# Kernel tuning notes

Measured on AMD Instinct MI355X. Metric: run time of the kernel, lower is better.

Reference implementation:

```python
import jax, jax.numpy as jnp
import numpy as np
import math

B, S, E, H, D, L, HF = 8, 1024, 512, 8, 64, 6, 2048
EPS = 1e-5
INF = 1000000.0


def _gelu(x):
    # custom tanh-approx gelu from the source
    return 0.5 * x * (1 + jnp.tanh(math.sqrt(2 / math.pi) * (x + 0.044715 * x ** 3)))


def _layernorm(x, gamma, beta):
    mean = jnp.mean(x, axis=-1, keepdims=True)
    var = jnp.mean((x - mean) ** 2, axis=-1, keepdims=True)
    return gamma * ((x - mean) / jnp.sqrt(var + EPS)) + beta


def setup_inputs() -> dict:
    key = jax.random.key(0)
    ks = jax.random.split(key, 10)
    scale = 0.02
    x = jax.random.normal(ks[0], (B, S, E), dtype=jnp.float32)
    att_mask = jax.random.randint(ks[1], (B, S), 0, 2) == 1
    WQ = jax.random.normal(ks[2], (L, E, E), dtype=jnp.float32) * scale
    WK = jax.random.normal(ks[3], (L, E, E), dtype=jnp.float32) * scale
    WV = jax.random.normal(ks[4], (L, E, E), dtype=jnp.float32) * scale
    WO = jax.random.normal(ks[5], (L, E, E), dtype=jnp.float32) * scale
    W1 = jax.random.normal(ks[6], (L, HF, E), dtype=jnp.float32) * scale
    W2 = jax.random.normal(ks[7], (L, E, HF), dtype=jnp.float32) * scale
    bQ = jnp.zeros((L, E)); bK = jnp.zeros((L, E)); bV = jnp.zeros((L, E)); bO = jnp.zeros((L, E))
    b1 = jnp.zeros((L, HF)); b2 = jnp.zeros((L, E))
    g1 = jnp.ones((L, E)); bt1 = jnp.zeros((L, E))
    g2 = jnp.ones((L, E)); bt2 = jnp.zeros((L, E))
    return {"x": x, "att_mask": att_mask, "WQ": WQ, "bQ": bQ, "WK": WK, "bK": bK,
            "WV": WV, "bV": bV, "WO": WO, "bO": bO, "W1": W1, "b1": b1, "W2": W2,
            "b2": b2, "g1": g1, "bt1": bt1, "g2": g2, "bt2": bt2}


def reference(x, att_mask, WQ, bQ, WK, bK, WV, bV, WO, bO, W1, b1, W2, b2, g1, bt1, g2, bt2):
    # additive mask applied to scores: score - (~mask) * infinity, broadcast over (B,1,1,S)
    inv_att = (~att_mask).astype(x.dtype)[:, None, None, :] * INF
    inv_sqrt_d = 1.0 / math.sqrt(D)
    for l in range(L):
        # --- multi-head self-attention ---
        q = (jnp.einsum('bse,fe->bsf', x, WQ[l]) + bQ[l]).reshape(B, S, H, D).transpose(0, 2, 1, 3)
        k = (jnp.einsum('bse,fe->bsf', x, WK[l]) + bK[l]).reshape(B, S, H, D).transpose(0, 2, 1, 3)
        v = (jnp.einsum('bse,fe->bsf', x, WV[l]) + bV[l]).reshape(B, S, H, D).transpose(0, 2, 1, 3)
        score = jnp.einsum('bhsd,bhtd->bhst', q, k) * inv_sqrt_d - inv_att
        attn = jax.nn.softmax(score, axis=-1)
        o = jnp.einsum('bhst,bhtd->bhsd', attn, v).transpose(0, 2, 1, 3).reshape(B, S, E)
        o = jnp.einsum('bse,fe->bsf', o, WO[l]) + bO[l]
        x = _layernorm(x + o, g1[l], bt1[l])
        # --- pointwise feed-forward ---
        h = _gelu(jnp.einsum('bse,fe->bsf', x, W1[l]) + b1[l])
        f = jnp.einsum('bsf,ef->bse', h, W2[l]) + b2[l]
        x = _layernorm(x + f, g2[l], bt2[l])
    return x
```

## Files before the change

kernel.cpp:

```cpp
#include <hip/hip_runtime.h>
#include <cstdint>
#include <cstddef>

#define NB 8
#define NS 1024
#define NE 512
#define NH 8
#define ND 64
#define NL 6
#define NHF 2048
#define NROW (NB*NS)

typedef __bf16 bf16_t;
typedef __bf16 bf8v __attribute__((ext_vector_type(8)));
typedef __bf16 bf4v __attribute__((ext_vector_type(4)));
typedef float  f4   __attribute__((ext_vector_type(4)));

extern "C" __device__ float __ocml_native_exp2_f32(float);
#define EXP2F __ocml_native_exp2_f32
#define LOG2E 1.4426950408889634f

__device__ __forceinline__ void async_copy16(const bf16_t* g, bf16_t* l) {
    __builtin_amdgcn_global_load_lds(
        (const __attribute__((address_space(1))) void*)g,
        (__attribute__((address_space(3))) void*)l,
        16, 0, 0);
}

__device__ __forceinline__ float gelu_f(float x) {
    const float s = fmaf(0.044715f * x * x, x, x);
    const float e = EXP2F(-2.3022081995f * s);
    return x * __builtin_amdgcn_rcpf(1.0f + e);
}

template<int BN, int ACT, int OUT>
__device__ __forceinline__ void gemm_core(
    bf16_t* __restrict__ sm,
    const bf16_t* __restrict__ A, const bf16_t* __restrict__ Bm,
    const float* __restrict__ bias, bf16_t* __restrict__ Cb,
    const unsigned short* __restrict__ rank,
    int m0, int n0, int N, int K)
{
    constexpr int JN = BN / 32, WSPAN = BN / 2;
    bf16_t* As = sm;
    bf16_t* Bs = sm + 2*128*64;
    const int tid  = threadIdx.x;
    const int lane = tid & 63;
    const int wave = tid >> 6;
    const int wm = wave >> 1, wn = wave & 1;
    const int quad = lane >> 4, l16 = lane & 15;
    const int srow = tid >> 3;
    const int scol = (((tid & 7) ^ (srow & 7)) << 3);

    f4 acc[4][JN] = {};

    const bf16_t* Ag = A  + (size_t)(m0 + srow) * K + scol;
    const bf16_t* Bg = Bm + (size_t)(n0 + srow) * K + scol;
    const int sw = (l16 & 7);

    auto stage = [&](int buf, int kt) {
#pragma unroll
        for (int r = 0; r < 4; ++r)
            async_copy16(Ag + (size_t)r * 32 * K + kt, As + buf*8192 + tid*8 + r*2048);
#pragma unroll
        for (int r = 0; r < BN/32; ++r)
            async_copy16(Bg + (size_t)r * 32 * K + kt, Bs + buf*(BN*64) + tid*8 + r*2048);
    };

    stage(0, 0);
    int buf = 0;
    for (int kt = 0; kt < K; kt += 64, buf ^= 1) {
        __syncthreads();
        if (kt + 64 < K) stage(buf ^ 1, kt + 64);
        const bf16_t* Ab = As + buf*8192;
        const bf16_t* Bb = Bs + buf*(BN*64);
#pragma unroll
        for (int s = 0; s < 2; ++s) {
            const int c8 = ((s*4 + quad) ^ sw) * 8;
            bf8v af[4], bfv[JN];
#pragma unroll
            for (int i = 0; i < 4; ++i)
                af[i] = *(const bf8v*)(Ab + (wm*64 + i*16 + l16)*64 + c8);
#pragma unroll
            for (int j = 0; j < JN; ++j)
                bfv[j] = *(const bf8v*)(Bb + (wn*WSPAN + j*16 + l16)*64 + c8);
#pragma unroll
            for (int i = 0; i < 4; ++i)
#pragma unroll
                for (int j = 0; j < JN; ++j) {
                    if (OUT == 5)
                        acc[i][j] = __builtin_amdgcn_mfma_f32_16x16x32_bf16(af[i], bfv[j], acc[i][j], 0, 0, 0);
                    else
                        acc[i][j] = __builtin_amdgcn_mfma_f32_16x16x32_bf16(bfv[j], af[i], acc[i][j], 0, 0, 0);
                }
        }
    }

    if (OUT != 5) {
#pragma unroll
        for (int i = 0; i < 4; ++i) {
            const int mi = m0 + wm*64 + i*16 + l16;
            size_t m = (size_t)mi;
            if (OUT == 4) m = (size_t)((mi & ~1023) + (int)rank[mi]);
#pragma unroll
            for (int j = 0; j < JN; ++j) {
                const int nb = n0 + wn*WSPAN + j*16 + quad*4;
                const f4 bv = *(const f4*)(bias + nb);
                f4 v = acc[i][j] + bv;
                if (ACT) {
#pragma unroll
                    for (int r = 0; r < 4; ++r) v[r] = gelu_f(v[r]);
                }
                bf4v* cp = (bf4v*)(Cb + m * (size_t)N + nb);
                bf4v o;
                if (OUT == 2) {
                    const bf4v old = *cp;
#pragma unroll
                    for (int r = 0; r < 4; ++r) o[r] = (bf16_t)((float)old[r] + v[r]);
                } else {
#pragma unroll
                    for (int r = 0; r < 4; ++r) o[r] = (bf16_t)v[r];
                }
                *cp = o;
            }
        }
    } else {
#pragma unroll
        for (int j = 0; j < JN; ++j) {
            const int n = n0 + wn*WSPAN + j*16 + l16;
            const float bv = bias[n];
#pragma unroll
            for (int i = 0; i < 4; ++i) {
                const int mbase = m0 + wm*64 + i*16 + quad*4;
                const size_t b8h = (size_t)((mbase >> 10)*8 + (n >> 6));
                bf16_t* rowp = Cb + (b8h*64 + (size_t)(n & 63))*1024;
#pragma unroll
                for (int r = 0; r < 4; ++r)
                    rowp[rank[mbase + r]] = (bf16_t)(acc[i][j][r] + bv);
            }
        }
    }
}

template<int BN, int ACT, int OUT>
__global__ __launch_bounds__(256)
void gemm_bt_k(const bf16_t* __restrict__ A, const bf16_t* __restrict__ Bm,
               const float* __restrict__ bias, bf16_t* __restrict__ Cb, int N, int K)
{
    __shared__ __align__(16) bf16_t smem[2*128*64 + 2*BN*64];
    gemm_core<BN, ACT, OUT>(smem, A, Bm, bias, Cb, nullptr,
                            blockIdx.x * 128, blockIdx.y * BN, N, K);
}

template<int ACT, int OUT>
__device__ __forceinline__ void gemm256_core(
    bf16_t* __restrict__ sm,
    const bf16_t* __restrict__ A, const bf16_t* __restrict__ Bm,
    const float* __restrict__ bias, bf16_t* __restrict__ Cb,
    const unsigned short* __restrict__ rank,
    int m0, int n0, int N, int K)
{
    const int tid  = threadIdx.x;
    const int lane = tid & 63;
    const int wave = tid >> 6;
    const int wm = wave >> 2, wn = wave & 3;
    const int quad = lane >> 4, l16 = lane & 15;
    const int sw = l16 & 7;
    const int srow = tid >> 3;
    const int scol = ((tid & 7) ^ (srow & 7)) << 3;

    bf16_t* As = sm;
    bf16_t* Bs = sm + 4 * 8192;

    const bf16_t* Ag = A  + (size_t)(m0 + srow) * K + scol;
    const bf16_t* Bg = Bm + (size_t)(n0 + srow) * K + scol;

    auto stageA = [&](int d, int h, int kt) {
        bf16_t* dst = As + (d*2 + h) * 8192 + tid * 8;
        const bf16_t* src = Ag + (size_t)(h * 128) * K + kt;
        async_copy16(src, dst);
        async_copy16(src + (size_t)64 * K, dst + 4096);
    };
    auto stageB = [&](int d, int h, int kt) {
        bf16_t* dst = Bs + (d*2 + h) * 8192 + tid * 8;
        const bf16_t* src = Bg + (size_t)(h * 128) * K + kt;
        async_copy16(src, dst);
        async_copy16(src + (size_t)64 * K, dst + 4096);
    };

    const int nt = K >> 6;

    f4 acc[8][4] = {};
    bf8v bfr[4][2], al[4][2], ah[4][2];

    auto mfmaQ = [&](const bf8v (&af)[4][2], int fb, int gb) {
#pragma unroll
        for (int kh = 0; kh < 2; ++kh)
#pragma unroll
            for (int f = 0; f < 4; ++f)
#pragma unroll
                for (int g = 0; g < 2; ++g) {
                    if (OUT == 5)
                        acc[fb+f][gb+g] = __builtin_amdgcn_mfma_f32_16x16x32_bf16(af[f][kh], bfr[gb+g][kh], acc[fb+f][gb+g], 0, 0, 0);
                    else
                        acc[fb+f][gb+g] = __builtin_amdgcn_mfma_f32_16x16x32_bf16(bfr[gb+g][kh], af[f][kh], acc[fb+f][gb+g], 0, 0, 0);
                }
    };

    stageB(0, 0, 0);  stageB(0, 1, 0);  stageA(0, 0, 0);  stageA(0, 1, 0);
    stageB(1, 0, 64); stageB(1, 1, 64); stageA(1, 0, 64);
    asm volatile("s_waitcnt vmcnt(6)" ::: "memory");
    __builtin_amdgcn_s_barrier();

    for (int t = 0; t < nt; ++t) {
        const int d = t & 1;
        const int kt2 = (t + 2) << 6;
        const bf16_t* Ab = As + (d*2 + wm) * 8192;
        const bf16_t* Bb = Bs + (d*2 + (wn >> 1)) * 8192 + (wn & 1) * 4096;

#pragma unroll
        for (int g = 0; g < 4; ++g)
#pragma unroll
            for (int kh = 0; kh < 2; ++kh)
                bfr[g][kh] = *(const bf8v*)(Bb + (g*16 + l16)*64 + (((kh*4 + quad) ^ sw) << 3));
#pragma unroll
        for (int f = 0; f < 4; ++f)
#pragma unroll
            for (int kh = 0; kh < 2; ++kh)
                al[f][kh] = *(const bf8v*)(Ab + (f*16 + l16)*64 + (((kh*4 + quad) ^ sw) << 3));
        if (t + 1 < nt) stageA(d ^ 1, 1, (t + 1) << 6);
        __builtin_amdgcn_s_barrier();
        __builtin_amdgcn_s_setprio(1);
        mfmaQ(al, 0, 0);
        __builtin_amdgcn_s_setprio(0);
        asm volatile("s_waitcnt lgkmcnt(0)" ::: "memory");
        __builtin_amdgcn_s_barrier();

#pragma unroll
        for (int f = 0; f < 4; ++f)
#pragma unroll
            for (int kh = 0; kh < 2; ++kh)
                ah[f][kh] = *(const bf8v*)(Ab + ((f + 4)*16 + l16)*64 + (((kh*4 + quad) ^ sw) << 3));
        if (t + 2 < nt) stageB(d, 0, kt2);
        __builtin_amdgcn_s_barrier();
        __builtin_amdgcn_s_setprio(1);
        mfmaQ(ah, 4, 0);
        __builtin_amdgcn_s_setprio(0);
        asm volatile("s_waitcnt lgkmcnt(0)" ::: "memory");
        __builtin_amdgcn_s_barrier();

        if (t + 2 < nt) stageB(d, 1, kt2);
        __builtin_amdgcn_s_barrier();
        __builtin_amdgcn_s_setprio(1);
        mfmaQ(al, 0, 2);
        __builtin_amdgcn_s_setprio(0);
        asm volatile("s_waitcnt lgkmcnt(0)" ::: "memory");
        __builtin_amdgcn_s_barrier();

        if (t + 2 < nt) stageA(d, 0, kt2);
        __builtin_amdgcn_s_barrier();
        __builtin_amdgcn_s_setprio(1);
        mfmaQ(ah, 4, 2);
        __builtin_amdgcn_s_setprio(0);
        asm volatile("s_waitcnt lgkmcnt(0)" ::: "memory");
        if (t + 1 < nt) {
            if (t + 2 < nt) asm volatile("s_waitcnt vmcnt(6)" ::: "memory");
            else            asm volatile("s_waitcnt vmcnt(0)" ::: "memory");
        }
        __builtin_amdgcn_s_barrier();
    }

    if (OUT != 5) {
#pragma unroll
        for (int f = 0; f < 8; ++f) {
            const int mi = m0 + wm*128 + f*16 + l16;
            size_t m = (size_t)mi;
            if (OUT == 4) m = (size_t)((mi & ~1023) + (int)rank[mi]);
#pragma unroll
            for (int g = 0; g < 4; ++g) {
                const int nb = n0 + wn*64 + g*16 + quad*4;
                const f4 bv = *(const f4*)(bias + nb);
                f4 v = acc[f][g] + bv;
                if (ACT) {
#pragma unroll
                    for (int r = 0; r < 4; ++r) v[r] = gelu_f(v[r]);
                }
                bf4v* cp = (bf4v*)(Cb + m * (size_t)N + nb);
                bf4v o;
                if (OUT == 2) {
                    const bf4v old = *cp;
#pragma unroll
                    for (int r = 0; r < 4; ++r) o[r] = (bf16_t)((float)old[r] + v[r]);
                } else {
#pragma unroll
                    for (int r = 0; r < 4; ++r) o[r] = (bf16_t)v[r];
                }
                *cp = o;
            }
        }
    } else {
#pragma unroll
        for (int g = 0; g < 4; ++g) {
            const int n = n0 + wn*64 + g*16 + l16;
            const float bv = bias[n];
#pragma unroll
            for (int f = 0; f < 8; ++f) {
                const int mbase = m0 + wm*128 + f*16 + quad*4;
                const size_t b8h = (size_t)((mbase >> 10)*8 + (n >> 6));
                bf16_t* rowp = Cb + (b8h*64 + (size_t)(n & 63))*1024;
#pragma unroll
                for (int r = 0; r < 4; ++r)
                    rowp[rank[mbase + r]] = (bf16_t)(acc[f][g][r] + bv);
            }
        }
    }
}

template<int ACT, int OUT>
__global__ __launch_bounds__(512, 2)
void gemm256_k(const bf16_t* __restrict__ A, const bf16_t* __restrict__ Bm,
               const float* __restrict__ bias, bf16_t* __restrict__ Cb, int N, int K)
{
    __shared__ __align__(16) bf16_t smem[8 * 8192];
    gemm256_core<ACT, OUT>(smem, A, Bm, bias, Cb, nullptr,
                           blockIdx.x * 256, blockIdx.y * 256, N, K);
}

__global__ __launch_bounds__(512, 2)
void gemm256_qkv_k(const bf16_t* __restrict__ A,
                   const bf16_t* __restrict__ wq, const bf16_t* __restrict__ wk, const bf16_t* __restrict__ wv,
                   const float* __restrict__ bq, const float* __restrict__ bk, const float* __restrict__ bv,
                   bf16_t* __restrict__ Q, bf16_t* __restrict__ K, bf16_t* __restrict__ Vt,
                   const unsigned short* __restrict__ rank)
{
    __shared__ __align__(16) bf16_t smem[8 * 8192];
    const int mat = blockIdx.y >> 1;
    const int m0 = blockIdx.x * 256, n0 = (blockIdx.y & 1) * 256;
    if (mat == 0)      gemm256_core<0, 1>(smem, A, wq, bq, Q,  nullptr, m0, n0, NE, NE);
    else if (mat == 1) gemm256_core<0, 4>(smem, A, wk, bk, K,  rank,    m0, n0, NE, NE);
    else               gemm256_core<0, 5>(smem, A, wv, bv, Vt, rank,    m0, n0, NE, NE);
}

__global__ __launch_bounds__(64)
void pack_k(const int* __restrict__ m, unsigned short* __restrict__ rank,
            int* __restrict__ cntpad, float* __restrict__ maskp)
{
    const int b = blockIdx.x, lane = threadIdx.x;
    unsigned long long bals[16];
    int cnt = 0;
#pragma unroll
    for (int c = 0; c < 16; ++c) {
        const bool mk = m[b*NS + c*64 + lane] != 0;
        bals[c] = __ballot(mk);
        cnt += __popcll(bals[c]);
    }
    int u = 0, kk = 0;
#pragma unroll
    for (int c = 0; c < 16; ++c) {
        const unsigned long long bal = bals[c];
        const bool mk = (bal >> lane) & 1;
        const int pu = __popcll(bal & ((1ull << lane) - 1));
        const int r = mk ? (u + pu) : (cnt + kk + (lane - pu));
        rank[b*NS + c*64 + lane] = (unsigned short)r;
        const int cb = __popcll(bal);
        u += cb; kk += 64 - cb;
    }
    if (lane == 0) {
        int cp = (cnt + 63) & ~63;
        cntpad[b] = cp < 64 ? 64 : cp;
    }
#pragma unroll
    for (int c = 0; c < 16; ++c) {
        const int j = c*64 + lane;
        maskp[b*NS + j] = (j < cnt) ? 0.0f : -1.0e6f * LOG2E;
    }
}

__global__ __launch_bounds__(256)
void attn_k(const bf16_t* __restrict__ Q, const bf16_t* __restrict__ Kg,
            const bf16_t* __restrict__ Vt, const float* __restrict__ maskf,
            const int* __restrict__ cntpad, bf16_t* __restrict__ O)
{
    __shared__ __align__(16) bf16_t Ks[2][64*64];
    __shared__ __align__(16) bf16_t Vs[2][64*64];
    __shared__ __align__(16) bf16_t Ps[4][32*64];
    const int tid  = threadIdx.x;
    const int lane = tid & 63;
    const int wave = tid >> 6;
    const int quad = lane >> 4, l16 = lane & 15;
    const int sw = l16 & 7;
    const int bh = blockIdx.x;
    const int b = bh >> 3, h = bh & 7;
    const int q0 = blockIdx.y * 128;
    const int kend = cntpad[b];

    bf8v qf[2][2];
#pragma unroll
    for (int qi = 0; qi < 2; ++qi) {
        const bf16_t* Qp = Q + (size_t)(b*NS + q0 + wave*32 + qi*16 + l16) * NE + h*ND;
        qf[qi][0] = *(const bf8v*)(Qp + quad*8);
        qf[qi][1] = *(const bf8v*)(Qp + 32 + quad*8);
    }

    f4 oacc[2][4] = {};
    float rs[2] = {0.f, 0.f};

    const int srow = tid >> 3;
    const int scol = (((tid & 7) ^ (srow & 7)) << 3);
    const float c1 = 0.125f * LOG2E;

    auto stage = [&](int buf, int kt) {
#pragma unroll
        for (int r = 0; r < 2; ++r) {
            async_copy16(Kg + (size_t)(b*NS + kt + r*32 + srow) * NE + h*ND + scol,
                         Ks[buf] + (r*256 + tid) * 8);
            async_copy16(Vt + (size_t)(bh*ND + r*32 + srow) * NS + kt + scol,
                         Vs[buf] + (r*256 + tid) * 8);
        }
    };

    stage(0, 0);
    int buf = 0;
    for (int kt = 0; kt < kend; kt += 64, buf ^= 1) {
        __syncthreads();
        if (kt + 64 < kend) stage(buf ^ 1, kt + 64);

        f4 sacc[2][4] = {};
        __builtin_amdgcn_s_setprio(1);
#pragma unroll
        for (int j = 0; j < 4; ++j) {
            bf8v kf0 = *(const bf8v*)(Ks[buf] + (j*16 + l16)*64 + ((quad    ) ^ sw)*8);
            bf8v kf1 = *(const bf8v*)(Ks[buf] + (j*16 + l16)*64 + ((quad + 4) ^ sw)*8);
#pragma unroll
            for (int qi = 0; qi < 2; ++qi) {
                sacc[qi][j] = __builtin_amdgcn_mfma_f32_16x16x32_bf16(kf0, qf[qi][0], sacc[qi][j], 0, 0, 0);
                sacc[qi][j] = __builtin_amdgcn_mfma_f32_16x16x32_bf16(kf1, qf[qi][1], sacc[qi][j], 0, 0, 0);
            }
        }
        __builtin_amdgcn_s_setprio(0);

        bf16_t* Pw = Ps[wave];
#pragma unroll
        for (int j = 0; j < 4; ++j) {
            const f4 mkv = *(const f4*)(maskf + b*NS + kt + j*16 + quad*4);
#pragma unroll
            for (int qi = 0; qi < 2; ++qi) {
                bf4v o;
#pragma unroll
                for (int r = 0; r < 4; ++r) {
                    const float p = EXP2F(fmaf(sacc[qi][j][r], c1, mkv[r]));
                    rs[qi] += p;
                    o[r] = (bf16_t)p;
                }
                const int row = qi*16 + l16;
                const int chunk = (j*2 + (quad >> 1)) ^ sw;
                *(bf4v*)(Pw + row*64 + chunk*8 + (quad & 1)*4) = o;
            }
        }

        __builtin_amdgcn_s_setprio(1);
#pragma unroll
        for (int ks = 0; ks < 2; ++ks) {
            bf8v pf[2];
#pragma unroll
            for (int qi = 0; qi < 2; ++qi)
                pf[qi] = *(const bf8v*)(Pw + (qi*16 + l16)*64 + ((ks*4 + quad) ^ sw)*8);
#pragma unroll
            for (int nt = 0; nt < 4; ++nt) {
                bf8v vf = *(const bf8v*)(Vs[buf] + (nt*16 + l16)*64 + ((ks*4 + quad) ^ sw)*8);
#pragma unroll
                for (int qi = 0; qi < 2; ++qi)
                    oacc[qi][nt] = __builtin_amdgcn_mfma_f32_16x16x32_bf16(vf, pf[qi], oacc[qi][nt], 0, 0, 0);
            }
        }
        __builtin_amdgcn_s_setprio(0);
    }

#pragma unroll
    for (int qi = 0; qi < 2; ++qi) {
        float s = rs[qi];
        s += __shfl_xor(s, 16, 64);
        s += __shfl_xor(s, 32, 64);
        const float inv = 1.0f / s;
        const size_t row = (size_t)(b*NS + q0 + wave*32 + qi*16 + l16);
#pragma unroll
        for (int nt = 0; nt < 4; ++nt) {
            bf4v o;
#pragma unroll
            for (int r = 0; r < 4; ++r) o[r] = (bf16_t)(oacc[qi][nt][r] * inv);
            *(bf4v*)(O + row * NE + h*ND + nt*16 + quad*4) = o;
        }
    }
}

__global__ __launch_bounds__(256)
void ln_k(bf16_t* __restrict__ xb,
          const float* __restrict__ gamma, const float* __restrict__ beta,
          float* __restrict__ fout, int wf)
{
    const int row = blockIdx.x;
    const int tid = threadIdx.x;
    const size_t base = (size_t)row * NE;
    const float x0 = (float)xb[base + tid];
    const float x1 = (float)xb[base + tid + 256];
    float s  = x0 + x1;
    float ss = x0*x0 + x1*x1;
#pragma unroll
    for (int off = 32; off > 0; off >>= 1) {
        s  += __shfl_down(s,  off, 64);
        ss += __shfl_down(ss, off, 64);
    }
    __shared__ float red[8];
    const int wave = tid >> 6;
    if ((tid & 63) == 0) { red[wave] = s; red[4 + wave] = ss; }
    __syncthreads();
    s  = red[0] + red[1] + red[2] + red[3];
    ss = red[4] + red[5] + red[6] + red[7];
    const float mean = s * (1.0f / NE);
    const float var  = ss * (1.0f / NE) - mean * mean;
    const float inv  = rsqrtf(var + 1e-5f);
    const float o0 = gamma[tid]       * ((x0 - mean) * inv) + beta[tid];
    const float o1 = gamma[tid + 256] * ((x1 - mean) * inv) + beta[tid + 256];
    xb[base + tid]       = (bf16_t)o0;
    xb[base + tid + 256] = (bf16_t)o1;
    if (wf) {
        fout[base + tid]       = o0;
        fout[base + tid + 256] = o1;
    }
}

#define W4SZ ((size_t)NL*NE*NE/4)
#define WBSZ ((size_t)NL*NE*NHF/4)
#define XSZ  ((size_t)NROW*NE/4)
#define CVT_TOTAL (4*W4SZ + 2*WBSZ + XSZ)

__global__ void cvt_all(const float* __restrict__ wq, const float* __restrict__ wk,
                        const float* __restrict__ wv, const float* __restrict__ wo,
                        const float* __restrict__ w1, const float* __restrict__ w2,
                        const float* __restrict__ x,
                        bf16_t* __restrict__ owq, bf16_t* __restrict__ owk,
                        bf16_t* __restrict__ owv, bf16_t* __restrict__ owo,
                        bf16_t* __restrict__ ow1, bf16_t* __restrict__ ow2,
                        bf16_t* __restrict__ ox)
{
    size_t i = (size_t)blockIdx.x * 256 + threadIdx.x;
    if (i >= CVT_TOTAL) return;
    const float* src; bf16_t* dst;
    if      (i < 1*W4SZ)           { src = wq; dst = owq; }
    else if (i < 2*W4SZ)           { src = wk; dst = owk; i -= 1*W4SZ; }
    else if (i < 3*W4SZ)           { src = wv; dst = owv; i -= 2*W4SZ; }
    else if (i < 4*W4SZ)           { src = wo; dst = owo; i -= 3*W4SZ; }
    else if (i < 4*W4SZ + WBSZ)    { src = w1; dst = ow1; i -= 4*W4SZ; }
    else if (i < 4*W4SZ + 2*WBSZ)  { src = w2; dst = ow2; i -= 4*W4SZ + WBSZ; }
    else                           { src = x;  dst = ox;  i -= 4*W4SZ + 2*WBSZ; }
    const f4 v = ((const f4*)src)[i];
    bf4v o;
    o[0] = (bf16_t)v[0]; o[1] = (bf16_t)v[1]; o[2] = (bf16_t)v[2]; o[3] = (bf16_t)v[3];
    ((bf4v*)dst)[i] = o;
}

extern "C" void kernel_launch(void* const* d_in, const int* in_sizes, int n_in,
                              void* d_out, int out_size, void* d_ws, size_t ws_size,
                              hipStream_t stream)
{
    (void)in_sizes; (void)n_in; (void)out_size; (void)ws_size;
    const float* x   = (const float*)d_in[0];
    const int*   msk = (const int*)d_in[1];
    const float* WQ = (const float*)d_in[2];  const float* bQ  = (const float*)d_in[3];
    const float* WK = (const float*)d_in[4];  const float* bK  = (const float*)d_in[5];
    const float* WV = (const float*)d_in[6];  const float* bV  = (const float*)d_in[7];
    const float* WO = (const float*)d_in[8];  const float* bO  = (const float*)d_in[9];
    const float* W1 = (const float*)d_in[10]; const float* b1  = (const float*)d_in[11];
    const float* W2 = (const float*)d_in[12]; const float* b2  = (const float*)d_in[13];
    const float* g1 = (const float*)d_in[14]; const float* bt1 = (const float*)d_in[15];
    const float* g2 = (const float*)d_in[16]; const float* bt2 = (const float*)d_in[17];

    char* ws = (char*)d_ws;
    size_t off = 0;
    auto alloc = [&](size_t bytes) { char* p = ws + off; off += (bytes + 255) & ~(size_t)255; return p; };
    bf16_t* xb    = (bf16_t*)alloc((size_t)NROW*NE*2);
    bf16_t* Qb    = (bf16_t*)alloc((size_t)NROW*NE*2);
    bf16_t* Kb    = (bf16_t*)alloc((size_t)NROW*NE*2);
    bf16_t* Vtb   = (bf16_t*)alloc((size_t)NROW*NE*2);
    bf16_t* AOb   = (bf16_t*)alloc((size_t)NROW*NE*2);
    bf16_t* hb    = (bf16_t*)alloc((size_t)NROW*NHF*2);
    bf16_t* wqc   = (bf16_t*)alloc((size_t)NL*NE*NE*2);
    bf16_t* wkc   = (bf16_t*)alloc((size_t)NL*NE*NE*2);
    bf16_t* wvc   = (bf16_t*)alloc((size_t)NL*NE*NE*2);
    bf16_t* woc   = (bf16_t*)alloc((size_t)NL*NE*NE*2);
    bf16_t* w1c   = (bf16_t*)alloc((size_t)NL*NHF*NE*2);
    bf16_t* w2c   = (bf16_t*)alloc((size_t)NL*NE*NHF*2);
    float*  maskp = (float*) alloc((size_t)NB*NS*4);
    unsigned short* rankb = (unsigned short*)alloc((size_t)NB*NS*2);
    int*    cntp  = (int*)   alloc(NB*4);

    cvt_all<<<dim3((unsigned)((CVT_TOTAL + 255) / 256)), dim3(256), 0, stream>>>(
        WQ, WK, WV, WO, W1, W2, x, wqc, wkc, wvc, woc, w1c, w2c, xb);
    pack_k<<<dim3(NB), dim3(64), 0, stream>>>(msk, rankb, cntp, maskp);

    for (int l = 0; l < NL; ++l) {
        const bf16_t* wq  = wqc + (size_t)l*NE*NE;
        const bf16_t* wk  = wkc + (size_t)l*NE*NE;
        const bf16_t* wv  = wvc + (size_t)l*NE*NE;
        const bf16_t* wo  = woc + (size_t)l*NE*NE;
        const bf16_t* w1p = w1c + (size_t)l*NHF*NE;
        const bf16_t* w2p = w2c + (size_t)l*NE*NHF;

        gemm256_qkv_k<<<dim3(32, 6), dim3(512), 0, stream>>>(
            xb, wq, wk, wv, bQ + l*NE, bK + l*NE, bV + l*NE, Qb, Kb, Vtb, rankb);
        attn_k<<<dim3(64, 8), dim3(256), 0, stream>>>(Qb, Kb, Vtb, maskp, cntp, AOb);
        gemm_bt_k<64, 0, 2><<<dim3(64, 8), dim3(256), 0, stream>>>(
            AOb, wo, bO + l*NE, xb, NE, NE);
        ln_k<<<dim3(NROW), dim3(256), 0, stream>>>(
            xb, g1 + l*NE, bt1 + l*NE, nullptr, 0);
        gemm256_k<1, 1><<<dim3(32, 8), dim3(512), 0, stream>>>(
            xb, w1p, b1 + l*NHF, hb, NHF, NE);
        gemm_bt_k<64, 0, 2><<<dim3(64, 8), dim3(256), 0, stream>>>(
            hb, w2p, b2 + l*NE, xb, NE, NHF);
        const int last = (l == NL - 1);
        ln_k<<<dim3(NROW), dim3(256), 0, stream>>>(
            xb, g2 + l*NE, bt2 + l*NE, (float*)d_out, last);
    }
}
```

Baseline: 1.039 ms.

## Split QKV into 128-tile GEMM plus separate V transpose kernel

Replaces the 256x256-tile fused QKV GEMM, whose V output went through a scattered per-element transposed store, with a 128x128-tile GEMM over 768 blocks. That GEMM writes V row-major (rank-permuted) into a new buffer. A new LDS-based transpose kernel then builds the V^T layout that attention expects, and it skips tiles beyond the padded count. The aim is to remove the uncoalesced 2-byte scatter writes and to give the grid more blocks. The cost is an extra kernel launch and an extra read and write of V.

New measurement: 949.8 us. -8.6%, faster.

```diff
diff --git a/kernel.cpp b/kernel.cpp
--- a/kernel.cpp
+++ b/kernel.cpp
@@ -87,57 +87,36 @@
 #pragma unroll
             for (int i = 0; i < 4; ++i)
 #pragma unroll
-                for (int j = 0; j < JN; ++j) {
-                    if (OUT == 5)
-                        acc[i][j] = __builtin_amdgcn_mfma_f32_16x16x32_bf16(af[i], bfv[j], acc[i][j], 0, 0, 0);
-                    else
-                        acc[i][j] = __builtin_amdgcn_mfma_f32_16x16x32_bf16(bfv[j], af[i], acc[i][j], 0, 0, 0);
-                }
-        }
-    }
-
-    if (OUT != 5) {
-#pragma unroll
-        for (int i = 0; i < 4; ++i) {
-            const int mi = m0 + wm*64 + i*16 + l16;
-            size_t m = (size_t)mi;
-            if (OUT == 4) m = (size_t)((mi & ~1023) + (int)rank[mi]);
-#pragma unroll
-            for (int j = 0; j < JN; ++j) {
-                const int nb = n0 + wn*WSPAN + j*16 + quad*4;
-                const f4 bv = *(const f4*)(bias + nb);
-                f4 v = acc[i][j] + bv;
-                if (ACT) {
-#pragma unroll
-                    for (int r = 0; r < 4; ++r) v[r] = gelu_f(v[r]);
-                }
-                bf4v* cp = (bf4v*)(Cb + m * (size_t)N + nb);
-                bf4v o;
-                if (OUT == 2) {
-                    const bf4v old = *cp;
-#pragma unroll
-                    for (int r = 0; r < 4; ++r) o[r] = (bf16_t)((float)old[r] + v[r]);
-                } else {
-#pragma unroll
-                    for (int r = 0; r < 4; ++r) o[r] = (bf16_t)v[r];
-                }
-                *cp = o;
+                for (int j = 0; j < JN; ++j)
+                    acc[i][j] = __builtin_amdgcn_mfma_f32_16x16x32_bf16(bfv[j], af[i], acc[i][j], 0, 0, 0);
+        }
+    }
+
+#pragma unroll
+    for (int i = 0; i < 4; ++i) {
+        const int mi = m0 + wm*64 + i*16 + l16;
+        size_t m = (size_t)mi;
+        if (OUT == 4) m = (size_t)((mi & ~1023) + (int)rank[mi]);
+#pragma unroll
+        for (int j = 0; j < JN; ++j) {
+            const int nb = n0 + wn*WSPAN + j*16 + quad*4;
+            const f4 bv = *(const f4*)(bias + nb);
+            f4 v = acc[i][j] + bv;
+            if (ACT) {
+#pragma unroll
+                for (int r = 0; r < 4; ++r) v[r] = gelu_f(v[r]);
             }
-        }
-    } else {
-#pragma unroll
-        for (int j = 0; j < JN; ++j) {
-            const int n = n0 + wn*WSPAN + j*16 + l16;
-            const float bv = bias[n];
-#pragma unroll
-            for (int i = 0; i < 4; ++i) {
-                const int mbase = m0 + wm*64 + i*16 + quad*4;
-                const size_t b8h = (size_t)((mbase >> 10)*8 + (n >> 6));
-                bf16_t* rowp = Cb + (b8h*64 + (size_t)(n & 63))*1024;
-#pragma unroll
-                for (int r = 0; r < 4; ++r)
-                    rowp[rank[mbase + r]] = (bf16_t)(acc[i][j][r] + bv);
+            bf4v* cp = (bf4v*)(Cb + m * (size_t)N + nb);
+            bf4v o;
+            if (OUT == 2) {
+                const bf4v old = *cp;
+#pragma unroll
+                for (int r = 0; r < 4; ++r) o[r] = (bf16_t)((float)old[r] + v[r]);
+            } else {
+#pragma unroll
+                for (int r = 0; r < 4; ++r) o[r] = (bf16_t)v[r];
             }
+            *cp = o;
         }
     }
 }
@@ -150,6 +129,49 @@
     __shared__ __align__(16) bf16_t smem[2*128*64 + 2*BN*64];
     gemm_core<BN, ACT, OUT>(smem, A, Bm, bias, Cb, nullptr,
                             blockIdx.x * 128, blockIdx.y * BN, N, K);
+}
+
+__global__ __launch_bounds__(256)
+void gemm_qkv_k(const bf16_t* __restrict__ A,
+                const bf16_t* __restrict__ wq, const bf16_t* __restrict__ wk, const bf16_t* __restrict__ wv,
+                const float* __restrict__ bq, const float* __restrict__ bk, const float* __restrict__ bv,
+                bf16_t* __restrict__ Q, bf16_t* __restrict__ K, bf16_t* __restrict__ Vp,
+                const unsigned short* __restrict__ rank)
+{
+    __shared__ __align__(16) bf16_t smem[2*128*64 + 2*128*64];
+    const int mat = blockIdx.y >> 2;
+    const int m0 = blockIdx.x * 128, n0 = (blockIdx.y & 3) * 128;
+    if (mat == 0)      gemm_core<128, 0, 1>(smem, A, wq, bq, Q,  nullptr, m0, n0, NE, NE);
+    else if (mat == 1) gemm_core<128, 0, 4>(smem, A, wk, bk, K,  rank,    m0, n0, NE, NE);
+    else               gemm_core<128, 0, 4>(smem, A, wv, bv, Vp, rank,    m0, n0, NE, NE);
+}
+
+__global__ __launch_bounds__(256)
+void vtp_k(const bf16_t* __restrict__ Vp, const int* __restrict__ cntpad,
+           bf16_t* __restrict__ Vt)
+{
+    const int bh = blockIdx.x, b = bh >> 3, h = bh & 7;
+    const int j0 = blockIdx.y * 64;
+    if (j0 >= cntpad[b]) return;
+    __shared__ __align__(16) bf16_t t[64][72];
+    const int tid = threadIdx.x;
+    const int jr = tid >> 3;
+    const int c8 = (tid & 7) * 8;
+#pragma unroll
+    for (int r = 0; r < 2; ++r) {
+        const int j = jr + r*32;
+        *(bf8v*)(&t[j][c8]) =
+            *(const bf8v*)(Vp + (size_t)(b*NS + j0 + j) * NE + h*ND + c8);
+    }
+    __syncthreads();
+#pragma unroll
+    for (int r = 0; r < 2; ++r) {
+        const int d = jr + r*32;
+        bf8v o;
+#pragma unroll
+        for (int u = 0; u < 8; ++u) o[u] = t[c8 + u][d];
+        *(bf8v*)(Vt + (size_t)(bh*ND + d) * NS + j0 + c8) = o;
+    }
 }
 
 template<int ACT, int OUT>
@@ -157,7 +179,6 @@
     bf16_t* __restrict__ sm,
     const bf16_t* __restrict__ A, const bf16_t* __restrict__ Bm,
     const float* __restrict__ bias, bf16_t* __restrict__ Cb,
-    const unsigned short* __restrict__ rank,
     int m0, int n0, int N, int K)
 {
     const int tid  = threadIdx.x;
@@ -199,12 +220,8 @@
 #pragma unroll
             for (int f = 0; f < 4; ++f)
 #pragma unroll
-                for (int g = 0; g < 2; ++g) {
-                    if (OUT == 5)
-                        acc[fb+f][gb+g] = __builtin_amdgcn_mfma_f32_16x16x32_bf16(af[f][kh], bfr[gb+g][kh], acc[fb+f][gb+g], 0, 0, 0);
-                    else
-                        acc[fb+f][gb+g] = __builtin_amdgcn_mfma_f32_16x16x32_bf16(bfr[gb+g][kh], af[f][kh], acc[fb+f][gb+g], 0, 0, 0);
-                }
+                for (int g = 0; g < 2; ++g)
+                    acc[fb+f][gb+g] = __builtin_amdgcn_mfma_f32_16x16x32_bf16(bfr[gb+g][kh], af[f][kh], acc[fb+f][gb+g], 0, 0, 0);
     };
 
     stageB(0, 0, 0);  stageB(0, 1, 0);  stageA(0, 0, 0);  stageA(0, 1, 0);
@@ -270,48 +287,30 @@
         __builtin_amdgcn_s_barrier();
     }
 
-    if (OUT != 5) {
-#pragma unroll
-        for (int f = 0; f < 8; ++f) {
-            const int mi = m0 + wm*128 + f*16 + l16;
-            size_t m = (size_t)mi;
-            if (OUT == 4) m = (size_t)((mi & ~1023) + (int)rank[mi]);
-#pragma unroll
-            for (int g = 0; g < 4; ++g) {
-                const int nb = n0 + wn*64 + g*16 + quad*4;
-                const f4 bv = *(const f4*)(bias + nb);
-                f4 v = acc[f][g] + bv;
-                if (ACT) {
-#pragma unroll
-                    for (int r = 0; r < 4; ++r) v[r] = gelu_f(v[r]);
-                }
-                bf4v* cp = (bf4v*)(Cb + m * (size_t)N + nb);
-                bf4v o;
-                if (OUT == 2) {
-                    const bf4v old = *cp;
-#pragma unroll
-                    for (int r = 0; r < 4; ++r) o[r] = (bf16_t)((float)old[r] + v[r]);
-                } else {
-#pragma unroll
-                    for (int r = 0; r < 4; ++r) o[r] = (bf16_t)v[r];
-                }
-                *cp = o;
+#pragma unroll
+    for (int f = 0; f < 8; ++f) {
+        const int mi = m0 + wm*128 + f*16 + l16;
+        const size_t m = (size_t)mi;
+#pragma unroll
+        for (int g = 0; g < 4; ++g) {
+            const int nb = n0 + wn*64 + g*16 + quad*4;
+            const f4 bv = *(const f4*)(bias + nb);
+            f4 v = acc[f][g] + bv;
+            if (ACT) {
+#pragma unroll
+                for (int r = 0; r < 4; ++r) v[r] = gelu_f(v[r]);
             }
-        }
-    } else {
-#pragma unroll
-        for (int g = 0; g < 4; ++g) {
-            const int n = n0 + wn*64 + g*16 + l16;
-            const float bv = bias[n];
-#pragma unroll
-            for (int f = 0; f < 8; ++f) {
-                const int mbase = m0 + wm*128 + f*16 + quad*4;
-                const size_t b8h = (size_t)((mbase >> 10)*8 + (n >> 6));
-                bf16_t* rowp = Cb + (b8h*64 + (size_t)(n & 63))*1024;
-#pragma unroll
-                for (int r = 0; r < 4; ++r)
-                    rowp[rank[mbase + r]] = (bf16_t)(acc[f][g][r] + bv);
+            bf4v* cp = (bf4v*)(Cb + m * (size_t)N + nb);
+            bf4v o;
+            if (OUT == 2) {
+                const bf4v old = *cp;
+#pragma unroll
+                for (int r = 0; r < 4; ++r) o[r] = (bf16_t)((float)old[r] + v[r]);
+            } else {
+#pragma unroll
+                for (int r = 0; r < 4; ++r) o[r] = (bf16_t)v[r];
             }
+            *cp = o;
         }
     }
 }
@@ -322,23 +321,8 @@
                const float* __restrict__ bias, bf16_t* __restrict__ Cb, int N, int K)
 {
     __shared__ __align__(16) bf16_t smem[8 * 8192];
-    gemm256_core<ACT, OUT>(smem, A, Bm, bias, Cb, nullptr,
+    gemm256_core<ACT, OUT>(smem, A, Bm, bias, Cb,
                            blockIdx.x * 256, blockIdx.y * 256, N, K);
-}
-
-__global__ __launch_bounds__(512, 2)
-void gemm256_qkv_k(const bf16_t* __restrict__ A,
-                   const bf16_t* __restrict__ wq, const bf16_t* __restrict__ wk, const bf16_t* __restrict__ wv,
-                   const float* __restrict__ bq, const float* __restrict__ bk, const float* __restrict__ bv,
-                   bf16_t* __restrict__ Q, bf16_t* __restrict__ K, bf16_t* __restrict__ Vt,
-                   const unsigned short* __restrict__ rank)
-{
-    __shared__ __align__(16) bf16_t smem[8 * 8192];
-    const int mat = blockIdx.y >> 1;
-    const int m0 = blockIdx.x * 256, n0 = (blockIdx.y & 1) * 256;
-    if (mat == 0)      gemm256_core<0, 1>(smem, A, wq, bq, Q,  nullptr, m0, n0, NE, NE);
-    else if (mat == 1) gemm256_core<0, 4>(smem, A, wk, bk, K,  rank,    m0, n0, NE, NE);
-    else               gemm256_core<0, 5>(smem, A, wv, bv, Vt, rank,    m0, n0, NE, NE);
 }
 
 __global__ __launch_bounds__(64)
@@ -581,6 +565,7 @@
     bf16_t* xb    = (bf16_t*)alloc((size_t)NROW*NE*2);
     bf16_t* Qb    = (bf16_t*)alloc((size_t)NROW*NE*2);
     bf16_t* Kb    = (bf16_t*)alloc((size_t)NROW*NE*2);
+    bf16_t* Vpb   = (bf16_t*)alloc((size_t)NROW*NE*2);
     bf16_t* Vtb   = (bf16_t*)alloc((size_t)NROW*NE*2);
     bf16_t* AOb   = (bf16_t*)alloc((size_t)NROW*NE*2);
     bf16_t* hb    = (bf16_t*)alloc((size_t)NROW*NHF*2);
@@ -606,8 +591,9 @@
         const bf16_t* w1p = w1c + (size_t)l*NHF*NE;
         const bf16_t* w2p = w2c + (size_t)l*NE*NHF;
 
-        gemm256_qkv_k<<<dim3(32, 6), dim3(512), 0, stream>>>(
-            xb, wq, wk, wv, bQ + l*NE, bK + l*NE, bV + l*NE, Qb, Kb, Vtb, rankb);
+        gemm_qkv_k<<<dim3(64, 12), dim3(256), 0, stream>>>(
+            xb, wq, wk, wv, bQ + l*NE, bK + l*NE, bV + l*NE, Qb, Kb, Vpb, rankb);
+        vtp_k<<<dim3(64, 16), dim3(256), 0, stream>>>(Vpb, cntp, Vtb);
         attn_k<<<dim3(64, 8), dim3(256), 0, stream>>>(Qb, Kb, Vtb, maskp, cntp, AOb);
         gemm_bt_k<64, 0, 2><<<dim3(64, 8), dim3(256), 0, stream>>>(
             AOb, wo, bO + l*NE, xb, NE, NE);
```

## Fuse QKV into one shared-A tile GEMM and stage 128-key chunks in attention

Applied to the files above, without the earlier changes.

Replaces the 256x256 QKV kernel, which split Q, K and V across separate blocks, with a 128x64-tile kernel. Each block stages the activation tile once and multiplies it against all three weight matrices, so A is reused and the grid grows to 512 blocks. The attention kernel now double-buffers 128 keys per barrier iteration, processed as two 64-key halves, which halves the number of syncs. In exchange it doubles K/V shared memory and adds register pressure from three accumulator sets, which may lower occupancy.

Result: faster. 930.3 us (-10.5%).

```diff
diff --git a/kernel.cpp b/kernel.cpp
--- a/kernel.cpp
+++ b/kernel.cpp
@@ -38,7 +38,6 @@
     bf16_t* __restrict__ sm,
     const bf16_t* __restrict__ A, const bf16_t* __restrict__ Bm,
     const float* __restrict__ bias, bf16_t* __restrict__ Cb,
-    const unsigned short* __restrict__ rank,
     int m0, int n0, int N, int K)
 {
     constexpr int JN = BN / 32, WSPAN = BN / 2;
@@ -87,57 +86,35 @@
 #pragma unroll
             for (int i = 0; i < 4; ++i)
 #pragma unroll
-                for (int j = 0; j < JN; ++j) {
-                    if (OUT == 5)
-                        acc[i][j] = __builtin_amdgcn_mfma_f32_16x16x32_bf16(af[i], bfv[j], acc[i][j], 0, 0, 0);
-                    else
-                        acc[i][j] = __builtin_amdgcn_mfma_f32_16x16x32_bf16(bfv[j], af[i], acc[i][j], 0, 0, 0);
-                }
-        }
-    }
-
-    if (OUT != 5) {
-#pragma unroll
-        for (int i = 0; i < 4; ++i) {
-            const int mi = m0 + wm*64 + i*16 + l16;
-            size_t m = (size_t)mi;
-            if (OUT == 4) m = (size_t)((mi & ~1023) + (int)rank[mi]);
-#pragma unroll
-            for (int j = 0; j < JN; ++j) {
-                const int nb = n0 + wn*WSPAN + j*16 + quad*4;
-                const f4 bv = *(const f4*)(bias + nb);
-                f4 v = acc[i][j] + bv;
-                if (ACT) {
-#pragma unroll
-                    for (int r = 0; r < 4; ++r) v[r] = gelu_f(v[r]);
-                }
-                bf4v* cp = (bf4v*)(Cb + m * (size_t)N + nb);
-                bf4v o;
-                if (OUT == 2) {
-                    const bf4v old = *cp;
-#pragma unroll
-                    for (int r = 0; r < 4; ++r) o[r] = (bf16_t)((float)old[r] + v[r]);
-                } else {
-#pragma unroll
-                    for (int r = 0; r < 4; ++r) o[r] = (bf16_t)v[r];
-                }
-                *cp = o;
+                for (int j = 0; j < JN; ++j)
+                    acc[i][j] = __builtin_amdgcn_mfma_f32_16x16x32_bf16(bfv[j], af[i], acc[i][j], 0, 0, 0);
+        }
+    }
+
+#pragma unroll
+    for (int i = 0; i < 4; ++i) {
+        const int mi = m0 + wm*64 + i*16 + l16;
+        const size_t m = (size_t)mi;
+#pragma unroll
+        for (int j = 0; j < JN; ++j) {
+            const int nb = n0 + wn*WSPAN + j*16 + quad*4;
+            const f4 bv = *(const f4*)(bias + nb);
+            f4 v = acc[i][j] + bv;
+            if (ACT) {
+#pragma unroll
+                for (int r = 0; r < 4; ++r) v[r] = gelu_f(v[r]);
             }
-        }
-    } else {
-#pragma unroll
-        for (int j = 0; j < JN; ++j) {
-            const int n = n0 + wn*WSPAN + j*16 + l16;
-            const float bv = bias[n];
-#pragma unroll
-            for (int i = 0; i < 4; ++i) {
-                const int mbase = m0 + wm*64 + i*16 + quad*4;
-                const size_t b8h = (size_t)((mbase >> 10)*8 + (n >> 6));
-                bf16_t* rowp = Cb + (b8h*64 + (size_t)(n & 63))*1024;
-#pragma unroll
-                for (int r = 0; r < 4; ++r)
-                    rowp[rank[mbase + r]] = (bf16_t)(acc[i][j][r] + bv);
+            bf4v* cp = (bf4v*)(Cb + m * (size_t)N + nb);
+            bf4v o;
+            if (OUT == 2) {
+                const bf4v old = *cp;
+#pragma unroll
+                for (int r = 0; r < 4; ++r) o[r] = (bf16_t)((float)old[r] + v[r]);
+            } else {
+#pragma unroll
+                for (int r = 0; r < 4; ++r) o[r] = (bf16_t)v[r];
             }
+            *cp = o;
         }
     }
 }
@@ -148,8 +125,113 @@
                const float* __restrict__ bias, bf16_t* __restrict__ Cb, int N, int K)
 {
     __shared__ __align__(16) bf16_t smem[2*128*64 + 2*BN*64];
-    gemm_core<BN, ACT, OUT>(smem, A, Bm, bias, Cb, nullptr,
+    gemm_core<BN, ACT, OUT>(smem, A, Bm, bias, Cb,
                             blockIdx.x * 128, blockIdx.y * BN, N, K);
+}
+
+__global__ __launch_bounds__(256, 2)
+void gemm_qkv_k(const bf16_t* __restrict__ A,
+                const bf16_t* __restrict__ wq, const bf16_t* __restrict__ wk, const bf16_t* __restrict__ wv,
+                const float* __restrict__ bq, const float* __restrict__ bk, const float* __restrict__ bv,
+                bf16_t* __restrict__ Q, bf16_t* __restrict__ K, bf16_t* __restrict__ Vt,
+                const unsigned short* __restrict__ rank)
+{
+    __shared__ __align__(16) bf16_t As_[2*128*64];
+    __shared__ __align__(16) bf16_t Bs_[3][2*64*64];
+    const int tid  = threadIdx.x;
+    const int lane = tid & 63;
+    const int wave = tid >> 6;
+    const int wm = wave >> 1, wn = wave & 1;
+    const int quad = lane >> 4, l16 = lane & 15;
+    const int sw = l16 & 7;
+    const int srow = tid >> 3;
+    const int scol = (((tid & 7) ^ (srow & 7)) << 3);
+    const int m0 = blockIdx.x * 128, n0 = blockIdx.y * 64;
+
+    const bf16_t* Ag = A + (size_t)(m0 + srow) * NE + scol;
+    const bf16_t* Wg0 = wq + (size_t)(n0 + srow) * NE + scol;
+    const bf16_t* Wg1 = wk + (size_t)(n0 + srow) * NE + scol;
+    const bf16_t* Wg2 = wv + (size_t)(n0 + srow) * NE + scol;
+
+    f4 acc[3][4][2] = {};
+
+    auto stage = [&](int buf, int kt) {
+#pragma unroll
+        for (int r = 0; r < 4; ++r)
+            async_copy16(Ag + (size_t)r*32*NE + kt, As_ + buf*8192 + tid*8 + r*2048);
+#pragma unroll
+        for (int r = 0; r < 2; ++r) {
+            async_copy16(Wg0 + (size_t)r*32*NE + kt, Bs_[0] + buf*4096 + tid*8 + r*2048);
+            async_copy16(Wg1 + (size_t)r*32*NE + kt, Bs_[1] + buf*4096 + tid*8 + r*2048);
+            async_copy16(Wg2 + (size_t)r*32*NE + kt, Bs_[2] + buf*4096 + tid*8 + r*2048);
+        }
+    };
+
+    stage(0, 0);
+    int buf = 0;
+    for (int kt = 0; kt < NE; kt += 64, buf ^= 1) {
+        __syncthreads();
+        if (kt + 64 < NE) stage(buf ^ 1, kt + 64);
+        const bf16_t* Ab = As_ + buf*8192;
+#pragma unroll
+        for (int s = 0; s < 2; ++s) {
+            const int c8 = ((s*4 + quad) ^ sw) * 8;
+            bf8v af[4];
+#pragma unroll
+            for (int i = 0; i < 4; ++i)
+                af[i] = *(const bf8v*)(Ab + (wm*64 + i*16 + l16)*64 + c8);
+#pragma unroll
+            for (int mat = 0; mat < 3; ++mat) {
+                const bf16_t* Bb = Bs_[mat] + buf*4096;
+                const bf8v b0 = *(const bf8v*)(Bb + (wn*32      + l16)*64 + c8);
+                const bf8v b1 = *(const bf8v*)(Bb + (wn*32 + 16 + l16)*64 + c8);
+                if (mat < 2) {
+#pragma unroll
+                    for (int i = 0; i < 4; ++i) {
+                        acc[mat][i][0] = __builtin_amdgcn_mfma_f32_16x16x32_bf16(b0, af[i], acc[mat][i][0], 0, 0, 0);
+                        acc[mat][i][1] = __builtin_amdgcn_mfma_f32_16x16x32_bf16(b1, af[i], acc[mat][i][1], 0, 0, 0);
+                    }
+                } else {
+#pragma unroll
+                    for (int i = 0; i < 4; ++i) {
+                        acc[2][i][0] = __builtin_amdgcn_mfma_f32_16x16x32_bf16(af[i], b0, acc[2][i][0], 0, 0, 0);
+                        acc[2][i][1] = __builtin_amdgcn_mfma_f32_16x16x32_bf16(af[i], b1, acc[2][i][1], 0, 0, 0);
+                    }
+                }
+            }
+        }
+    }
+
+#pragma unroll
+    for (int i = 0; i < 4; ++i) {
+        const int mi = m0 + wm*64 + i*16 + l16;
+        const int mk = (mi & ~1023) + (int)rank[mi];
+#pragma unroll
+        for (int j = 0; j < 2; ++j) {
+            const int nb = n0 + wn*32 + j*16 + quad*4;
+            const f4 vq = acc[0][i][j] + *(const f4*)(bq + nb);
+            const f4 vk = acc[1][i][j] + *(const f4*)(bk + nb);
+            bf4v oq, ok;
+#pragma unroll
+            for (int r = 0; r < 4; ++r) { oq[r] = (bf16_t)vq[r]; ok[r] = (bf16_t)vk[r]; }
+            *(bf4v*)(Q + (size_t)mi * NE + nb) = oq;
+            *(bf4v*)(K + (size_t)mk * NE + nb) = ok;
+        }
+    }
+#pragma unroll
+    for (int j = 0; j < 2; ++j) {
+        const int n = n0 + wn*32 + j*16 + l16;
+        const float bvv = bv[n];
+#pragma unroll
+        for (int i = 0; i < 4; ++i) {
+            const int mbase = m0 + wm*64 + i*16 + quad*4;
+            const size_t b8h = (size_t)((mbase >> 10)*8 + (n >> 6));
+            bf16_t* rowp = Vt + (b8h*64 + (size_t)(n & 63))*1024;
+#pragma unroll
+            for (int r = 0; r < 4; ++r)
+                rowp[rank[mbase + r]] = (bf16_t)(acc[2][i][j][r] + bvv);
+        }
+    }
 }
 
 template<int ACT, int OUT>
@@ -157,7 +239,6 @@
     bf16_t* __restrict__ sm,
     const bf16_t* __restrict__ A, const bf16_t* __restrict__ Bm,
     const float* __restrict__ bias, bf16_t* __restrict__ Cb,
-    const unsigned short* __restrict__ rank,
     int m0, int n0, int N, int K)
 {
     const int tid  = threadIdx.x;
@@ -199,12 +280,8 @@
 #pragma unroll
             for (int f = 0; f < 4; ++f)
 #pragma unroll
-                for (int g = 0; g < 2; ++g) {
-                    if (OUT == 5)
-                        acc[fb+f][gb+g] = __builtin_amdgcn_mfma_f32_16x16x32_bf16(af[f][kh], bfr[gb+g][kh], acc[fb+f][gb+g], 0, 0, 0);
-                    else
-                        acc[fb+f][gb+g] = __builtin_amdgcn_mfma_f32_16x16x32_bf16(bfr[gb+g][kh], af[f][kh], acc[fb+f][gb+g], 0, 0, 0);
-                }
+                for (int g = 0; g < 2; ++g)
+                    acc[fb+f][gb+g] = __builtin_amdgcn_mfma_f32_16x16x32_bf16(bfr[gb+g][kh], af[f][kh], acc[fb+f][gb+g], 0, 0, 0);
     };
 
     stageB(0, 0, 0);  stageB(0, 1, 0);  stageA(0, 0, 0);  stageA(0, 1, 0);
@@ -270,48 +347,30 @@
         __builtin_amdgcn_s_barrier();
     }
 
-    if (OUT != 5) {
-#pragma unroll
-        for (int f = 0; f < 8; ++f) {
-            const int mi = m0 + wm*128 + f*16 + l16;
-            size_t m = (size_t)mi;
-            if (OUT == 4) m = (size_t)((mi & ~1023) + (int)rank[mi]);
-#pragma unroll
-            for (int g = 0; g < 4; ++g) {
-                const int nb = n0 + wn*64 + g*16 + quad*4;
-                const f4 bv = *(const f4*)(bias + nb);
-                f4 v = acc[f][g] + bv;
-                if (ACT) {
-#pragma unroll
-                    for (int r = 0; r < 4; ++r) v[r] = gelu_f(v[r]);
-                }
-                bf4v* cp = (bf4v*)(Cb + m * (size_t)N + nb);
-                bf4v o;
-                if (OUT == 2) {
-                    const bf4v old = *cp;
-#pragma unroll
-                    for (int r = 0; r < 4; ++r) o[r] = (bf16_t)((float)old[r] + v[r]);
-                } else {
-#pragma unroll
-                    for (int r = 0; r < 4; ++r) o[r] = (bf16_t)v[r];
-                }
-                *cp = o;
+#pragma unroll
+    for (int f = 0; f < 8; ++f) {
+        const int mi = m0 + wm*128 + f*16 + l16;
+        const size_t m = (size_t)mi;
+#pragma unroll
+        for (int g = 0; g < 4; ++g) {
+            const int nb = n0 + wn*64 + g*16 + quad*4;
+            const f4 bv = *(const f4*)(bias + nb);
+            f4 v = acc[f][g] + bv;
+            if (ACT) {
+#pragma unroll
+                for (int r = 0; r < 4; ++r) v[r] = gelu_f(v[r]);
             }
-        }
-    } else {
-#pragma unroll
-        for (int g = 0; g < 4; ++g) {
-            const int n = n0 + wn*64 + g*16 + l16;
-            const float bv = bias[n];
-#pragma unroll
-            for (int f = 0; f < 8; ++f) {
-                const int mbase = m0 + wm*128 + f*16 + quad*4;
-                const size_t b8h = (size_t)((mbase >> 10)*8 + (n >> 6));
-                bf16_t* rowp = Cb + (b8h*64 + (size_t)(n & 63))*1024;
-#pragma unroll
-                for (int r = 0; r < 4; ++r)
-                    rowp[rank[mbase + r]] = (bf16_t)(acc[f][g][r] + bv);
+            bf4v* cp = (bf4v*)(Cb + m * (size_t)N + nb);
+            bf4v o;
+            if (OUT == 2) {
+                const bf4v old = *cp;
+#pragma unroll
+                for (int r = 0; r < 4; ++r) o[r] = (bf16_t)((float)old[r] + v[r]);
+            } else {
+#pragma unroll
+                for (int r = 0; r < 4; ++r) o[r] = (bf16_t)v[r];
             }
+            *cp = o;
         }
     }
 }
@@ -322,23 +381,8 @@
                const float* __restrict__ bias, bf16_t* __restrict__ Cb, int N, int K)
 {
     __shared__ __align__(16) bf16_t smem[8 * 8192];
-    gemm256_core<ACT, OUT>(smem, A, Bm, bias, Cb, nullptr,
+    gemm256_core<ACT, OUT>(smem, A, Bm, bias, Cb,
                            blockIdx.x * 256, blockIdx.y * 256, N, K);
-}
-
-__global__ __launch_bounds__(512, 2)
-void gemm256_qkv_k(const bf16_t* __restrict__ A,
-                   const bf16_t* __restrict__ wq, const bf16_t* __restrict__ wk, const bf16_t* __restrict__ wv,
-                   const float* __restrict__ bq, const float* __restrict__ bk, const float* __restrict__ bv,
-                   bf16_t* __restrict__ Q, bf16_t* __restrict__ K, bf16_t* __restrict__ Vt,
-                   const unsigned short* __restrict__ rank)
-{
-    __shared__ __align__(16) bf16_t smem[8 * 8192];
-    const int mat = blockIdx.y >> 1;
-    const int m0 = blockIdx.x * 256, n0 = (blockIdx.y & 1) * 256;
-    if (mat == 0)      gemm256_core<0, 1>(smem, A, wq, bq, Q,  nullptr, m0, n0, NE, NE);
-    else if (mat == 1) gemm256_core<0, 4>(smem, A, wk, bk, K,  rank,    m0, n0, NE, NE);
-    else               gemm256_core<0, 5>(smem, A, wv, bv, Vt, rank,    m0, n0, NE, NE);
 }
 
 __global__ __launch_bounds__(64)
@@ -381,8 +425,8 @@
             const bf16_t* __restrict__ Vt, const float* __restrict__ maskf,
             const int* __restrict__ cntpad, bf16_t* __restrict__ O)
 {
-    __shared__ __align__(16) bf16_t Ks[2][64*64];
-    __shared__ __align__(16) bf16_t Vs[2][64*64];
+    __shared__ __align__(16) bf16_t Ks[2][2][64*64];
+    __shared__ __align__(16) bf16_t Vs[2][2][64*64];
     __shared__ __align__(16) bf16_t Ps[4][32*64];
     const int tid  = threadIdx.x;
     const int lane = tid & 63;
@@ -390,14 +434,14 @@
     const int quad = lane >> 4, l16 = lane & 15;
     const int sw = l16 & 7;
     const int bh = blockIdx.x;
-    const int b = bh >> 3, h = bh & 7;
+    const int b = bh >> 3, hd = bh & 7;
     const int q0 = blockIdx.y * 128;
     const int kend = cntpad[b];
 
     bf8v qf[2][2];
 #pragma unroll
     for (int qi = 0; qi < 2; ++qi) {
-        const bf16_t* Qp = Q + (size_t)(b*NS + q0 + wave*32 + qi*16 + l16) * NE + h*ND;
+        const bf16_t* Qp = Q + (size_t)(b*NS + q0 + wave*32 + qi*16 + l16) * NE + hd*ND;
         qf[qi][0] = *(const bf8v*)(Qp + quad*8);
         qf[qi][1] = *(const bf8v*)(Qp + 32 + quad*8);
     }
@@ -411,69 +455,80 @@
 
     auto stage = [&](int buf, int kt) {
 #pragma unroll
-        for (int r = 0; r < 2; ++r) {
-            async_copy16(Kg + (size_t)(b*NS + kt + r*32 + srow) * NE + h*ND + scol,
-                         Ks[buf] + (r*256 + tid) * 8);
-            async_copy16(Vt + (size_t)(bh*ND + r*32 + srow) * NS + kt + scol,
-                         Vs[buf] + (r*256 + tid) * 8);
-        }
+        for (int hh = 0; hh < 2; ++hh)
+#pragma unroll
+            for (int r = 0; r < 2; ++r) {
+                async_copy16(Kg + (size_t)(b*NS + kt + hh*64 + r*32 + srow) * NE + hd*ND + scol,
+                             Ks[buf][hh] + (r*256 + tid) * 8);
+                async_copy16(Vt + (size_t)(bh*ND + r*32 + srow) * NS + kt + hh*64 + scol,
+                             Vs[buf][hh] + (r*256 + tid) * 8);
+            }
     };
 
     stage(0, 0);
     int buf = 0;
-    for (int kt = 0; kt < kend; kt += 64, buf ^= 1) {
+    for (int kt = 0; kt < kend; kt += 128, buf ^= 1) {
         __syncthreads();
-        if (kt + 64 < kend) stage(buf ^ 1, kt + 64);
-
-        f4 sacc[2][4] = {};
-        __builtin_amdgcn_s_setprio(1);
-#pragma unroll
-        for (int j = 0; j < 4; ++j) {
-            bf8v kf0 = *(const bf8v*)(Ks[buf] + (j*16 + l16)*64 + ((quad    ) ^ sw)*8);
-            bf8v kf1 = *(const bf8v*)(Ks[buf] + (j*16 + l16)*64 + ((quad + 4) ^ sw)*8);
-#pragma unroll
-            for (int qi = 0; qi < 2; ++qi) {
-                sacc[qi][j] = __builtin_amdgcn_mfma_f32_16x16x32_bf16(kf0, qf[qi][0], sacc[qi][j], 0, 0, 0);
-                sacc[qi][j] = __builtin_amdgcn_mfma_f32_16x16x32_bf16(kf1, qf[qi][1], sacc[qi][j], 0, 0, 0);
+        if (kt + 128 < kend) stage(buf ^ 1, kt + 128);
+
+#pragma unroll
+        for (int hh = 0; hh < 2; ++hh) {
+            const int k0 = kt + hh*64;
+            if (k0 < kend) {
+                const bf16_t* Kb = Ks[buf][hh];
+                const bf16_t* Vb = Vs[buf][hh];
+
+                f4 sacc[2][4] = {};
+                __builtin_amdgcn_s_setprio(1);
+#pragma unroll
+                for (int j = 0; j < 4; ++j) {
+                    bf8v kf0 = *(const bf8v*)(Kb + (j*16 + l16)*64 + ((quad    ) ^ sw)*8);
+                    bf8v kf1 = *(const bf8v*)(Kb + (j*16 + l16)*64 + ((quad + 4) ^ sw)*8);
+#pragma unroll
+                    for (int qi = 0; qi < 2; ++qi) {
+                        sacc[qi][j] = __builtin_amdgcn_mfma_f32_16x16x32_bf16(kf0, qf[qi][0], sacc[qi][j], 0, 0, 0);
+                        sacc[qi][j] = __builtin_amdgcn_mfma_f32_16x16x32_bf16(kf1, qf[qi][1], sacc[qi][j], 0, 0, 0);
+                    }
+                }
+                __builtin_amdgcn_s_setprio(0);
+
+                bf16_t* Pw = Ps[wave];
+#pragma unroll
+                for (int j = 0; j < 4; ++j) {
+                    const f4 mkv = *(const f4*)(maskf + b*NS + k0 + j*16 + quad*4);
+#pragma unroll
+                    for (int qi = 0; qi < 2; ++qi) {
+                        bf4v o;
+#pragma unroll
+                        for (int r = 0; r < 4; ++r) {
+                            const float p = EXP2F(fmaf(sacc[qi][j][r], c1, mkv[r]));
+                            rs[qi] += p;
+                            o[r] = (bf16_t)p;
+                        }
+                        const int row = qi*16 + l16;
+                        const int chunk = (j*2 + (quad >> 1)) ^ sw;
+                        *(bf4v*)(Pw + row*64 + chunk*8 + (quad & 1)*4) = o;
+                    }
+                }
+
+                __builtin_amdgcn_s_setprio(1);
+#pragma unroll
+                for (int ks = 0; ks < 2; ++ks) {
+                    bf8v pf[2];
+#pragma unroll
+                    for (int qi = 0; qi < 2; ++qi)
+                        pf[qi] = *(const bf8v*)(Pw + (qi*16 + l16)*64 + ((ks*4 + quad) ^ sw)*8);
+#pragma unroll
+                    for (int nt = 0; nt < 4; ++nt) {
+                        bf8v vf = *(const bf8v*)(Vb + (nt*16 + l16)*64 + ((ks*4 + quad) ^ sw)*8);
+#pragma unroll
+                        for (int qi = 0; qi < 2; ++qi)
+                            oacc[qi][nt] = __builtin_amdgcn_mfma_f32_16x16x32_bf16(vf, pf[qi], oacc[qi][nt], 0, 0, 0);
+                    }
+                }
+                __builtin_amdgcn_s_setprio(0);
             }
         }
-        __builtin_amdgcn_s_setprio(0);
-
-        bf16_t* Pw = Ps[wave];
-#pragma unroll
-        for (int j = 0; j < 4; ++j) {
-            const f4 mkv = *(const f4*)(maskf + b*NS + kt + j*16 + quad*4);
-#pragma unroll
-            for (int qi = 0; qi < 2; ++qi) {
-                bf4v o;
-#pragma unroll
-                for (int r = 0; r < 4; ++r) {
-                    const float p = EXP2F(fmaf(sacc[qi][j][r], c1, mkv[r]));
-                    rs[qi] += p;
-                    o[r] = (bf16_t)p;
-                }
-                const int row = qi*16 + l16;
-                const int chunk = (j*2 + (quad >> 1)) ^ sw;
-                *(bf4v*)(Pw + row*64 + chunk*8 + (quad & 1)*4) = o;
-            }
-        }
-
-        __builtin_amdgcn_s_setprio(1);
-#pragma unroll
-        for (int ks = 0; ks < 2; ++ks) {
-            bf8v pf[2];
-#pragma unroll
-            for (int qi = 0; qi < 2; ++qi)
-                pf[qi] = *(const bf8v*)(Pw + (qi*16 + l16)*64 + ((ks*4 + quad) ^ sw)*8);
-#pragma unroll
-            for (int nt = 0; nt < 4; ++nt) {
-                bf8v vf = *(const bf8v*)(Vs[buf] + (nt*16 + l16)*64 + ((ks*4 + quad) ^ sw)*8);
-#pragma unroll
-                for (int qi = 0; qi < 2; ++qi)
-                    oacc[qi][nt] = __builtin_amdgcn_mfma_f32_16x16x32_bf16(vf, pf[qi], oacc[qi][nt], 0, 0, 0);
-            }
-        }
-        __builtin_amdgcn_s_setprio(0);
     }
 
 #pragma unroll
@@ -488,7 +543,7 @@
             bf4v o;
 #pragma unroll
             for (int r = 0; r < 4; ++r) o[r] = (bf16_t)(oacc[qi][nt][r] * inv);
-            *(bf4v*)(O + row * NE + h*ND + nt*16 + quad*4) = o;
+            *(bf4v*)(O + row * NE + hd*ND + nt*16 + quad*4) = o;
         }
     }
 }
@@ -606,7 +661,7 @@
         const bf16_t* w1p = w1c + (size_t)l*NHF*NE;
         const bf16_t* w2p = w2c + (size_t)l*NE*NHF;
 
-        gemm256_qkv_k<<<dim3(32, 6), dim3(512), 0, stream>>>(
+        gemm_qkv_k<<<dim3(64, 8), dim3(256), 0, stream>>>(
             xb, wq, wk, wv, bQ + l*NE, bK + l*NE, bV + l*NE, Qb, Kb, Vtb, rankb);
         attn_k<<<dim3(64, 8), dim3(256), 0, stream>>>(Qb, Kb, Vtb, maskp, cntp, AOb);
         gemm_bt_k<64, 0, 2><<<dim3(64, 8), dim3(256), 0, stream>>>(
```
